# Performance work log

Hardware: AMD Instinct MI355X
Metric: run time of the kernel (lower is better)

The kernel has to match this reference:

```python
import jax, jax.numpy as jnp
import numpy as np

# TASK_EMBEDDING_MAP from the original module, in ALL_TASKS order:
# ContributionRepo, PRReviewer, RepoMaintainer, SimDeveloper
ALL_TASK_ENTS = [
    ["contributor", "repository"],
    ["repository", "pr", "contributor"],
    ["repository", "contributor"],
    ["contributor", "contributor"],
]

B, IN, D = 131072, 256, 64


def setup_inputs() -> dict:
    key = jax.random.key(0)
    ks = jax.random.split(key, 64)

    def nrm(k, shape):
        return (jax.random.normal(k, shape) * 0.02).astype(jnp.float32)

    inp = {}
    task_idx = jax.random.randint(ks[0], (B,), 0, 4)
    inp["task_one_hot"] = jax.nn.one_hot(task_idx, 4, dtype=jnp.float32)
    for j, nm in enumerate(["c_x", "r_x", "p_x", "i_x"]):
        inp[nm] = jax.random.normal(ks[1 + j], (B, IN), dtype=jnp.float32)
    # entity embedding linears: Linear(IN, D) -> weight [D, IN], bias [D]
    kk = 5
    for nm in ["c", "r", "p", "i"]:
        inp["w_" + nm] = nrm(ks[kk], (D, IN)); kk += 1
        inp["b_" + nm] = jnp.zeros((D,), jnp.float32)
    # per-task MLPs: Linear(D*k, 512) -> ReLU -> Linear(512, 128) -> ReLU -> Linear(128, 1) -> Sigmoid
    for t, ents in enumerate(ALL_TASK_ENTS):
        din = D * len(ents)
        inp[f"w1_{t}"] = nrm(ks[kk], (512, din)); kk += 1
        inp[f"b1_{t}"] = jnp.zeros((512,), jnp.float32)
        inp[f"w2_{t}"] = nrm(ks[kk], (128, 512)); kk += 1
        inp[f"b2_{t}"] = jnp.zeros((128,), jnp.float32)
        inp[f"w3_{t}"] = nrm(ks[kk], (1, 128)); kk += 1
        inp[f"b3_{t}"] = jnp.zeros((1,), jnp.float32)
    return inp


def _forward(task_one_hot, c_x, r_x, p_x, i_x,
             w_c, b_c, w_r, b_r, w_p, b_p, w_i, b_i, task_params):
    # entity embedding linears (issue is computed as in the original, even if unused by tasks)
    e = {
        "contributor": c_x @ w_c.T + b_c,
        "repository": r_x @ w_r.T + b_r,
        "pr": p_x @ w_p.T + b_p,
        "issue": i_x @ w_i.T + b_i,
    }
    idx = jnp.argmax(task_one_hot, axis=1)  # [B], same as torch.max(..., dim=1).indices
    # Run every task MLP over the full batch (4 fixed experts), then select per-sample.
    outs = []
    for (w1, b1, w2, b2, w3, b3), ents in zip(task_params, ALL_TASK_ENTS):
        x = jnp.concatenate([e[n] for n in ents], axis=-1)  # [B, D*k]
        h = jax.nn.relu(x @ w1.T + b1)   # [B, 512]
        h = jax.nn.relu(h @ w2.T + b2)   # [B, 128]
        outs.append(jax.nn.sigmoid(h @ w3.T + b3)[:, 0])  # [B]
    all_out = jnp.stack(outs, axis=1)  # [B, 4]
    return jnp.take_along_axis(all_out, idx[:, None], axis=1)[:, 0]  # [B], matches x.squeeze()


def reference(task_one_hot, c_x, r_x, p_x, i_x,
              w_c, b_c, w_r, b_r, w_p, b_p, w_i, b_i,
              w1_0, b1_0, w2_0, b2_0, w3_0, b3_0,
              w1_1, b1_1, w2_1, b2_1, w3_1, b3_1,
              w1_2, b1_2, w2_2, b2_2, w3_2, b3_2,
              w1_3, b1_3, w2_3, b2_3, w3_3, b3_3):
    tp = [
        (w1_0, b1_0, w2_0, b2_0, w3_0, b3_0),
        (w1_1, b1_1, w2_1, b2_1, w3_1, b3_1),
        (w1_2, b1_2, w2_2, b2_2, w3_2, b3_2),
        (w1_3, b1_3, w2_3, b2_3, w3_3, b3_3),
    ]
    return _forward(task_one_hot, c_x, r_x, p_x, i_x,
                    w_c, b_c, w_r, b_r, w_p, b_p, w_i, b_i, tp)
```

## Files before the change

kernel.cpp:

```cpp
#include <hip/hip_runtime.h>
#include <stdint.h>

#define B_N 131072
#define IN_DIM 256

typedef __attribute__((ext_vector_type(8))) short bhalf8;
typedef __attribute__((ext_vector_type(4))) float f32x4;

__device__ constexpr int kW1Off[4] = {49152, 114688, 212992, 278528};
#define W2_OFF 344064
#define PREP_TOTAL 606208

__device__ __forceinline__ short f2bf(float x) {
    unsigned u = __float_as_uint(x);
    unsigned r = (u + 0x7fffu + ((u >> 16) & 1u)) >> 16;
    return (short)r;
}

struct PrepParams {
    const float* src[11];
    short* dst;
    int* cnt;
};

__global__ void prep_kernel(PrepParams P) {
    const int seg[11] = {16384,16384,16384, 65536,98304,65536,65536, 65536,65536,65536,65536};
    int g = blockIdx.x * blockDim.x + threadIdx.x;
    if (g < 4) P.cnt[g] = 0;
    const int stride = gridDim.x * blockDim.x;
    for (int i = g; i < PREP_TOTAL; i += stride) {
        int s = 0, base = 0;
        #pragma unroll
        for (int k = 0; k < 10; ++k) {
            if (i >= base + seg[k]) { base += seg[k]; s = k + 1; }
        }
        P.dst[i] = f2bf(P.src[s][i - base]);
    }
}

__global__ void partition_kernel(const float* __restrict__ oh, int* cnt, int* lists) {
    int i = blockIdx.x * 256 + threadIdx.x;
    const int lane = threadIdx.x & 63;
    bool valid = i < B_N;
    int t = -1;
    if (valid) {
        f32x4 v = *(const f32x4*)(oh + 4 * (size_t)i);
        t = 0; float best = v.x;
        if (v.y > best) { best = v.y; t = 1; }
        if (v.z > best) { best = v.z; t = 2; }
        if (v.w > best) { best = v.w; t = 3; }
    }
    #pragma unroll
    for (int tt = 0; tt < 4; ++tt) {
        unsigned long long m = __ballot(t == tt);
        if (m == 0ull) continue;
        int leader = __ffsll((unsigned long long)m) - 1;
        int base = 0;
        if (lane == leader) base = atomicAdd(&cnt[tt], __popcll(m));
        base = __shfl(base, leader);
        if (t == tt) {
            int pos = base + __popcll(m & ((1ull << lane) - 1ull));
            lists[tt * B_N + pos] = i;
        }
    }
}

struct MlpParams {
    const float* xs[3];
    const float* bes[3];
    const float* b1[4];
    const float* b2[4];
    const float* b3[4];
    const float* w3f[4];
    const short* bf;
    const int* cnt;
    const int* lists;
    float* out;
};

#define PA 200
#define PH 520

template<int TASK>
__device__ __forceinline__ void mlp_body(const MlpParams& P, short* sA, short* sH,
                                         int* sIdx, float* sRed, int m_count, int tile0) {
    constexpr int NS  = (TASK == 1) ? 3 : 2;
    constexpr int DIN = 64 * NS;
    constexpr int KS1 = DIN / 32;
    constexpr int SL0 = (TASK == 0) ? 0 : (TASK == 1) ? 1 : (TASK == 2) ? 1 : 0;
    constexpr int SL1 = (TASK == 0) ? 1 : (TASK == 1) ? 2 : (TASK == 2) ? 0 : 0;
    constexpr int SL2 = 0;

    const int tid  = threadIdx.x;
    const int wave = tid >> 6;
    const int lane = tid & 63;
    const int quad = lane >> 4;
    const int l16  = lane & 15;

    if (tid < 64) {
        int gp = tile0 + tid;
        int cl = gp < m_count ? gp : (m_count - 1);
        sIdx[tid] = P.lists[TASK * B_N + cl];
    }
    __syncthreads();

    #pragma unroll
    for (int pass = 0; pass < (NS * 4 + 7) / 8; ++pass) {
        int u = wave + pass * 8;
        if (u < NS * 4) {
            const int slot = u >> 2;
            const int mt   = u & 3;
            const int ent  = (slot == 0) ? SL0 : (slot == 1) ? SL1 : SL2;
            const float* xrow = P.xs[ent] + (size_t)sIdx[mt * 16 + l16] * IN_DIM;
            const float* be   = P.bes[ent];
            const short* we   = P.bf + ent * 16384;

            bhalf8 af[8];
            #pragma unroll
            for (int ks = 0; ks < 8; ++ks) {
                const int k0 = ks * 32 + quad * 8;
                f32x4 x0 = *(const f32x4*)(xrow + k0);
                f32x4 x1 = *(const f32x4*)(xrow + k0 + 4);
                bhalf8 f;
                f[0] = f2bf(x0.x); f[1] = f2bf(x0.y); f[2] = f2bf(x0.z); f[3] = f2bf(x0.w);
                f[4] = f2bf(x1.x); f[5] = f2bf(x1.y); f[6] = f2bf(x1.z); f[7] = f2bf(x1.w);
                af[ks] = f;
            }
            #pragma unroll
            for (int nt = 0; nt < 4; ++nt) {
                const int n = nt * 16 + l16;
                f32x4 acc = {0.f, 0.f, 0.f, 0.f};
                #pragma unroll
                for (int ks = 0; ks < 8; ++ks) {
                    bhalf8 bv = *(const bhalf8*)(we + n * 256 + ks * 32 + quad * 8);
                    acc = __builtin_amdgcn_mfma_f32_16x16x32_bf16(af[ks], bv, acc, 0, 0, 0);
                }
                const float bias = be[n];
                #pragma unroll
                for (int r = 0; r < 4; ++r) {
                    sA[(mt * 16 + quad * 4 + r) * PA + slot * 64 + n] = f2bf(acc[r] + bias);
                }
            }
        }
    }
    __syncthreads();

    {
        const short* w1 = P.bf + kW1Off[TASK];
        const float* b1 = P.b1[TASK];
        bhalf8 af[4][KS1];
        #pragma unroll
        for (int mt = 0; mt < 4; ++mt)
            #pragma unroll
            for (int ks = 0; ks < KS1; ++ks)
                af[mt][ks] = *(const bhalf8*)(sA + (mt * 16 + l16) * PA + ks * 32 + quad * 8);

        #pragma unroll
        for (int ntl = 0; ntl < 4; ++ntl) {
            const int n = (wave * 4 + ntl) * 16 + l16;
            f32x4 acc[4];
            #pragma unroll
            for (int mt = 0; mt < 4; ++mt) acc[mt] = {0.f, 0.f, 0.f, 0.f};
            #pragma unroll
            for (int ks = 0; ks < KS1; ++ks) {
                bhalf8 bv = *(const bhalf8*)(w1 + n * DIN + ks * 32 + quad * 8);
                #pragma unroll
                for (int mt = 0; mt < 4; ++mt)
                    acc[mt] = __builtin_amdgcn_mfma_f32_16x16x32_bf16(af[mt][ks], bv, acc[mt], 0, 0, 0);
            }
            const float bias = b1[n];
            #pragma unroll
            for (int mt = 0; mt < 4; ++mt)
                #pragma unroll
                for (int r = 0; r < 4; ++r) {
                    float v = acc[mt][r] + bias;
                    v = v > 0.f ? v : 0.f;
                    sH[(mt * 16 + quad * 4 + r) * PH + n] = f2bf(v);
                }
        }
    }
    __syncthreads();

    {
        const short* w2 = P.bf + W2_OFF + TASK * 65536;
        const float* b2 = P.b2[TASK];
        const float* w3 = P.w3f[TASK];
        const int mt = wave & 3;
        const int nh = wave >> 2;

        bhalf8 a2[16];
        #pragma unroll
        for (int ks = 0; ks < 16; ++ks)
            a2[ks] = *(const bhalf8*)(sH + (mt * 16 + l16) * PH + ks * 32 + quad * 8);

        float s0 = 0.f, s1 = 0.f, s2 = 0.f, s3 = 0.f;
        #pragma unroll
        for (int ntl = 0; ntl < 4; ++ntl) {
            const int n = (nh * 4 + ntl) * 16 + l16;
            f32x4 acc = {0.f, 0.f, 0.f, 0.f};
            #pragma unroll
            for (int ks = 0; ks < 16; ++ks) {
                bhalf8 bv = *(const bhalf8*)(w2 + n * 512 + ks * 32 + quad * 8);
                acc = __builtin_amdgcn_mfma_f32_16x16x32_bf16(a2[ks], bv, acc, 0, 0, 0);
            }
            const float bias = b2[n];
            const float wv = w3[n];
            float h;
            h = acc[0] + bias; h = h > 0.f ? h : 0.f; s0 += h * wv;
            h = acc[1] + bias; h = h > 0.f ? h : 0.f; s1 += h * wv;
            h = acc[2] + bias; h = h > 0.f ? h : 0.f; s2 += h * wv;
            h = acc[3] + bias; h = h > 0.f ? h : 0.f; s3 += h * wv;
        }
        #pragma unroll
        for (int m = 1; m < 16; m <<= 1) {
            s0 += __shfl_xor(s0, m);
            s1 += __shfl_xor(s1, m);
            s2 += __shfl_xor(s2, m);
            s3 += __shfl_xor(s3, m);
        }
        if (l16 == 0) {
            const int rbase = mt * 16 + quad * 4;
            sRed[(rbase + 0) * 2 + nh] = s0;
            sRed[(rbase + 1) * 2 + nh] = s1;
            sRed[(rbase + 2) * 2 + nh] = s2;
            sRed[(rbase + 3) * 2 + nh] = s3;
        }
    }
    __syncthreads();

    if (tid < 64) {
        int gp = tile0 + tid;
        if (gp < m_count) {
            float z = sRed[tid * 2] + sRed[tid * 2 + 1] + P.b3[TASK][0];
            float o = 1.0f / (1.0f + expf(-z));
            P.out[sIdx[tid]] = o;
        }
    }
}

__global__ __launch_bounds__(512)
void mlp_kernel(MlpParams P) {
    __shared__ short sA[64 * PA];
    __shared__ short sH[64 * PH];
    __shared__ int   sIdx[64];
    __shared__ float sRed[128];

    const int task  = blockIdx.y;
    const int tile0 = blockIdx.x * 64;
    const int m_count = P.cnt[task];
    if (tile0 >= m_count) return;

    switch (task) {
        case 0: mlp_body<0>(P, sA, sH, sIdx, sRed, m_count, tile0); break;
        case 1: mlp_body<1>(P, sA, sH, sIdx, sRed, m_count, tile0); break;
        case 2: mlp_body<2>(P, sA, sH, sIdx, sRed, m_count, tile0); break;
        default: mlp_body<3>(P, sA, sH, sIdx, sRed, m_count, tile0); break;
    }
}

extern "C" void kernel_launch(void* const* d_in, const int* in_sizes, int n_in,
                              void* d_out, int out_size, void* d_ws, size_t ws_size,
                              hipStream_t stream) {
    int*   cnt   = (int*)d_ws;
    int*   lists = (int*)((char*)d_ws + 64);
    short* bf    = (short*)((char*)d_ws + 64 + (size_t)4 * B_N * 4);

    PrepParams pp;
    pp.src[0]  = (const float*)d_in[5];
    pp.src[1]  = (const float*)d_in[7];
    pp.src[2]  = (const float*)d_in[9];
    pp.src[3]  = (const float*)d_in[13];
    pp.src[4]  = (const float*)d_in[19];
    pp.src[5]  = (const float*)d_in[25];
    pp.src[6]  = (const float*)d_in[31];
    pp.src[7]  = (const float*)d_in[15];
    pp.src[8]  = (const float*)d_in[21];
    pp.src[9]  = (const float*)d_in[27];
    pp.src[10] = (const float*)d_in[33];
    pp.dst = bf;
    pp.cnt = cnt;
    prep_kernel<<<512, 256, 0, stream>>>(pp);

    partition_kernel<<<(B_N + 255) / 256, 256, 0, stream>>>((const float*)d_in[0], cnt, lists);

    MlpParams mp;
    mp.xs[0]  = (const float*)d_in[1];
    mp.xs[1]  = (const float*)d_in[2];
    mp.xs[2]  = (const float*)d_in[3];
    mp.bes[0] = (const float*)d_in[6];
    mp.bes[1] = (const float*)d_in[8];
    mp.bes[2] = (const float*)d_in[10];
    for (int t = 0; t < 4; ++t) {
        mp.b1[t]  = (const float*)d_in[14 + 6 * t];
        mp.b2[t]  = (const float*)d_in[16 + 6 * t];
        mp.w3f[t] = (const float*)d_in[17 + 6 * t];
        mp.b3[t]  = (const float*)d_in[18 + 6 * t];
    }
    mp.bf    = bf;
    mp.cnt   = cnt;
    mp.lists = lists;
    mp.out   = (float*)d_out;

    mlp_kernel<<<dim3((B_N + 63) / 64, 4), 512, 0, stream>>>(mp);
}
```

Baseline: 772.0 us.

## Interleave layer1 and layer2 in 128-column chunks and cut shared memory

Splits the 512-wide hidden layer into four 128-column chunks held in double-buffered shared memory. Layer 2 consumes the previous chunk while layer 1 produces the next, which shrinks sH and register pressure, and launch bounds now request 4 blocks per CU for occupancy. Task 3 computes the contributor embedding once and duplicates it into both slots instead of running the same embedding twice. The partition kernel now aggregates per-block counts in shared memory so it issues fewer global atomics. In exchange there are more block-wide syncs, and A operands are reloaded from LDS each chunk.

After: 655.8 us. 1.18x faster.

```diff
diff --git a/kernel.cpp b/kernel.cpp
--- a/kernel.cpp
+++ b/kernel.cpp
@@ -38,28 +38,37 @@
     }
 }
 
-__global__ void partition_kernel(const float* __restrict__ oh, int* cnt, int* lists) {
-    int i = blockIdx.x * 256 + threadIdx.x;
-    const int lane = threadIdx.x & 63;
-    bool valid = i < B_N;
-    int t = -1;
-    if (valid) {
-        f32x4 v = *(const f32x4*)(oh + 4 * (size_t)i);
-        t = 0; float best = v.x;
-        if (v.y > best) { best = v.y; t = 1; }
-        if (v.z > best) { best = v.z; t = 2; }
-        if (v.w > best) { best = v.w; t = 3; }
-    }
+__global__ __launch_bounds__(1024)
+void partition_kernel(const float* __restrict__ oh, int* cnt, int* lists) {
+    __shared__ int sCnt[4];
+    __shared__ int sWOff[16][4];
+    __shared__ int sBase[4];
+    const int tid  = threadIdx.x;
+    const int wave = tid >> 6;
+    const int lane = tid & 63;
+    const int i = blockIdx.x * 1024 + tid;
+
+    f32x4 v = *(const f32x4*)(oh + 4 * (size_t)i);
+    int t = 0; float best = v.x;
+    if (v.y > best) { best = v.y; t = 1; }
+    if (v.z > best) { best = v.z; t = 2; }
+    if (v.w > best) { best = v.w; t = 3; }
+
+    if (tid < 4) sCnt[tid] = 0;
+    __syncthreads();
     #pragma unroll
     for (int tt = 0; tt < 4; ++tt) {
-        unsigned long long m = __ballot(t == tt);
-        if (m == 0ull) continue;
-        int leader = __ffsll((unsigned long long)m) - 1;
-        int base = 0;
-        if (lane == leader) base = atomicAdd(&cnt[tt], __popcll(m));
-        base = __shfl(base, leader);
+        unsigned long long mk = __ballot(t == tt);
+        if (lane == 0) sWOff[wave][tt] = mk ? atomicAdd(&sCnt[tt], __popcll(mk)) : 0;
+    }
+    __syncthreads();
+    if (tid < 4) sBase[tid] = atomicAdd(&cnt[tid], sCnt[tid]);
+    __syncthreads();
+    #pragma unroll
+    for (int tt = 0; tt < 4; ++tt) {
+        unsigned long long mk = __ballot(t == tt);
         if (t == tt) {
-            int pos = base + __popcll(m & ((1ull << lane) - 1ull));
+            int pos = sBase[tt] + sWOff[wave][tt] + __popcll(mk & ((1ull << lane) - 1ull));
             lists[tt * B_N + pos] = i;
         }
     }
@@ -78,8 +87,8 @@
     float* out;
 };
 
-#define PA 200
-#define PH 520
+#define PA  200
+#define PHC 136
 
 template<int TASK>
 __device__ __forceinline__ void mlp_body(const MlpParams& P, short* sA, short* sH,
@@ -90,6 +99,7 @@
     constexpr int SL0 = (TASK == 0) ? 0 : (TASK == 1) ? 1 : (TASK == 2) ? 1 : 0;
     constexpr int SL1 = (TASK == 0) ? 1 : (TASK == 1) ? 2 : (TASK == 2) ? 0 : 0;
     constexpr int SL2 = 0;
+    constexpr int NUNITS = (TASK == 3) ? 4 : NS * 4;
 
     const int tid  = threadIdx.x;
     const int wave = tid >> 6;
@@ -105,9 +115,9 @@
     __syncthreads();
 
     #pragma unroll
-    for (int pass = 0; pass < (NS * 4 + 7) / 8; ++pass) {
+    for (int pass = 0; pass < (NUNITS + 7) / 8; ++pass) {
         int u = wave + pass * 8;
-        if (u < NS * 4) {
+        if (u < NUNITS) {
             const int slot = u >> 2;
             const int mt   = u & 3;
             const int ent  = (slot == 0) ? SL0 : (slot == 1) ? SL1 : SL2;
@@ -138,78 +148,90 @@
                 const float bias = be[n];
                 #pragma unroll
                 for (int r = 0; r < 4; ++r) {
-                    sA[(mt * 16 + quad * 4 + r) * PA + slot * 64 + n] = f2bf(acc[r] + bias);
+                    const short val = f2bf(acc[r] + bias);
+                    const int row = mt * 16 + quad * 4 + r;
+                    sA[row * PA + slot * 64 + n] = val;
+                    if (TASK == 3) sA[row * PA + 64 + n] = val;
                 }
             }
         }
     }
     __syncthreads();
 
-    {
-        const short* w1 = P.bf + kW1Off[TASK];
-        const float* b1 = P.b1[TASK];
-        bhalf8 af[4][KS1];
-        #pragma unroll
-        for (int mt = 0; mt < 4; ++mt)
-            #pragma unroll
-            for (int ks = 0; ks < KS1; ++ks)
-                af[mt][ks] = *(const bhalf8*)(sA + (mt * 16 + l16) * PA + ks * 32 + quad * 8);
-
-        #pragma unroll
-        for (int ntl = 0; ntl < 4; ++ntl) {
-            const int n = (wave * 4 + ntl) * 16 + l16;
-            f32x4 acc[4];
-            #pragma unroll
-            for (int mt = 0; mt < 4; ++mt) acc[mt] = {0.f, 0.f, 0.f, 0.f};
+    const short* w1 = P.bf + kW1Off[TASK];
+    const float* b1 = P.b1[TASK];
+    const short* w2 = P.bf + W2_OFF + TASK * 65536;
+    const int mt4 = wave & 3;
+    const int nh  = wave >> 2;
+
+    f32x4 acc2[4];
+    #pragma unroll
+    for (int ntl = 0; ntl < 4; ++ntl) acc2[ntl] = {0.f, 0.f, 0.f, 0.f};
+
+    #pragma unroll
+    for (int cc = 0; cc <= 4; ++cc) {
+        bhalf8 a2[4];
+        if (cc >= 1) {
+            const short* hb = sH + ((cc - 1) & 1) * (64 * PHC);
+            #pragma unroll
+            for (int ks = 0; ks < 4; ++ks)
+                a2[ks] = *(const bhalf8*)(hb + (mt4 * 16 + l16) * PHC + ks * 32 + quad * 8);
+        }
+        if (cc < 4) {
+            short* hb = sH + (cc & 1) * (64 * PHC);
+            const int nl = wave * 16 + l16;
+            const int n  = cc * 128 + nl;
+            f32x4 acc1[4];
+            #pragma unroll
+            for (int mt = 0; mt < 4; ++mt) acc1[mt] = {0.f, 0.f, 0.f, 0.f};
             #pragma unroll
             for (int ks = 0; ks < KS1; ++ks) {
                 bhalf8 bv = *(const bhalf8*)(w1 + n * DIN + ks * 32 + quad * 8);
                 #pragma unroll
-                for (int mt = 0; mt < 4; ++mt)
-                    acc[mt] = __builtin_amdgcn_mfma_f32_16x16x32_bf16(af[mt][ks], bv, acc[mt], 0, 0, 0);
+                for (int mt = 0; mt < 4; ++mt) {
+                    bhalf8 av = *(const bhalf8*)(sA + (mt * 16 + l16) * PA + ks * 32 + quad * 8);
+                    acc1[mt] = __builtin_amdgcn_mfma_f32_16x16x32_bf16(av, bv, acc1[mt], 0, 0, 0);
+                }
             }
             const float bias = b1[n];
             #pragma unroll
             for (int mt = 0; mt < 4; ++mt)
                 #pragma unroll
                 for (int r = 0; r < 4; ++r) {
-                    float v = acc[mt][r] + bias;
+                    float v = acc1[mt][r] + bias;
                     v = v > 0.f ? v : 0.f;
-                    sH[(mt * 16 + quad * 4 + r) * PH + n] = f2bf(v);
-                }
-        }
-    }
-    __syncthreads();
+                    hb[(mt * 16 + quad * 4 + r) * PHC + nl] = f2bf(v);
+                }
+        }
+        if (cc >= 1) {
+            const int c0 = (cc - 1) * 128;
+            #pragma unroll
+            for (int ntl = 0; ntl < 4; ++ntl) {
+                const int n2 = (nh * 4 + ntl) * 16 + l16;
+                #pragma unroll
+                for (int ks = 0; ks < 4; ++ks) {
+                    bhalf8 bv = *(const bhalf8*)(w2 + n2 * 512 + c0 + ks * 32 + quad * 8);
+                    acc2[ntl] = __builtin_amdgcn_mfma_f32_16x16x32_bf16(a2[ks], bv, acc2[ntl], 0, 0, 0);
+                }
+            }
+        }
+        __syncthreads();
+    }
 
     {
-        const short* w2 = P.bf + W2_OFF + TASK * 65536;
         const float* b2 = P.b2[TASK];
         const float* w3 = P.w3f[TASK];
-        const int mt = wave & 3;
-        const int nh = wave >> 2;
-
-        bhalf8 a2[16];
-        #pragma unroll
-        for (int ks = 0; ks < 16; ++ks)
-            a2[ks] = *(const bhalf8*)(sH + (mt * 16 + l16) * PH + ks * 32 + quad * 8);
-
         float s0 = 0.f, s1 = 0.f, s2 = 0.f, s3 = 0.f;
         #pragma unroll
         for (int ntl = 0; ntl < 4; ++ntl) {
-            const int n = (nh * 4 + ntl) * 16 + l16;
-            f32x4 acc = {0.f, 0.f, 0.f, 0.f};
-            #pragma unroll
-            for (int ks = 0; ks < 16; ++ks) {
-                bhalf8 bv = *(const bhalf8*)(w2 + n * 512 + ks * 32 + quad * 8);
-                acc = __builtin_amdgcn_mfma_f32_16x16x32_bf16(a2[ks], bv, acc, 0, 0, 0);
-            }
-            const float bias = b2[n];
-            const float wv = w3[n];
+            const int n2 = (nh * 4 + ntl) * 16 + l16;
+            const float bias = b2[n2];
+            const float wv = w3[n2];
             float h;
-            h = acc[0] + bias; h = h > 0.f ? h : 0.f; s0 += h * wv;
-            h = acc[1] + bias; h = h > 0.f ? h : 0.f; s1 += h * wv;
-            h = acc[2] + bias; h = h > 0.f ? h : 0.f; s2 += h * wv;
-            h = acc[3] + bias; h = h > 0.f ? h : 0.f; s3 += h * wv;
+            h = acc2[ntl][0] + bias; h = h > 0.f ? h : 0.f; s0 += h * wv;
+            h = acc2[ntl][1] + bias; h = h > 0.f ? h : 0.f; s1 += h * wv;
+            h = acc2[ntl][2] + bias; h = h > 0.f ? h : 0.f; s2 += h * wv;
+            h = acc2[ntl][3] + bias; h = h > 0.f ? h : 0.f; s3 += h * wv;
         }
         #pragma unroll
         for (int m = 1; m < 16; m <<= 1) {
@@ -219,7 +241,7 @@
             s3 += __shfl_xor(s3, m);
         }
         if (l16 == 0) {
-            const int rbase = mt * 16 + quad * 4;
+            const int rbase = mt4 * 16 + quad * 4;
             sRed[(rbase + 0) * 2 + nh] = s0;
             sRed[(rbase + 1) * 2 + nh] = s1;
             sRed[(rbase + 2) * 2 + nh] = s2;
@@ -238,10 +260,10 @@
     }
 }
 
-__global__ __launch_bounds__(512)
+__global__ __launch_bounds__(512, 4)
 void mlp_kernel(MlpParams P) {
     __shared__ short sA[64 * PA];
-    __shared__ short sH[64 * PH];
+    __shared__ short sH[2 * 64 * PHC];
     __shared__ int   sIdx[64];
     __shared__ float sRed[128];
 
@@ -281,7 +303,7 @@
     pp.cnt = cnt;
     prep_kernel<<<512, 256, 0, stream>>>(pp);
 
-    partition_kernel<<<(B_N + 255) / 256, 256, 0, stream>>>((const float*)d_in[0], cnt, lists);
+    partition_kernel<<<B_N / 1024, 1024, 0, stream>>>((const float*)d_in[0], cnt, lists);
 
     MlpParams mp;
     mp.xs[0]  = (const float*)d_in[1];
```
